# Optimization experiments

Hardware: AMD Instinct MI355X
Metric: run time of the kernel (lower is better)

The kernel has to match this reference:

```python
import jax, jax.numpy as jnp
import numpy as np

SH_C0 = 0.28209479177387814
EPS2D = 0.3      # gsplat low-pass filter added to 2D covariance diagonal
NEAR = 0.01
ALPHA_MIN = 1.0 / 255.0
ALPHA_MAX = 0.999


def setup_inputs() -> dict:
    key = jax.random.key(0)
    ks = jax.random.split(key, 5)
    N = 2048
    means = 0.1 * jax.random.normal(ks[0], (N, 3), jnp.float32)
    quats = jax.random.normal(ks[1], (N, 4), jnp.float32)
    scales = -2.3 + 0.3 * jax.random.normal(ks[2], (N, 3), jnp.float32)
    opacities = -1.0 + 0.5 * jax.random.normal(ks[3], (N,), jnp.float32)
    sh_coeffs = jax.random.normal(ks[4], (N, 1, 3), jnp.float32)
    viewmats = jnp.eye(4, dtype=jnp.float32).at[2, 3].set(2.0)[None]  # [1,4,4] world->cam
    Ks = jnp.array([[[150.0, 0.0, 64.0], [0.0, 150.0, 64.0], [0.0, 0.0, 1.0]]], jnp.float32)
    return dict(means=means, quats=quats, scales=scales, opacities=opacities,
                sh_coeffs=sh_coeffs, viewmats=viewmats, Ks=Ks, width=128, height=128)


def _splat_render(means, quats, scales, opacities, sh_coeffs, viewmats, Ks, width, height):
    # --- parameter activations (GaussianSplat.activated_parameters) ---
    quats = quats / jnp.linalg.norm(quats, axis=-1, keepdims=True)
    scales = jnp.minimum(jnp.exp(scales), 10.0)
    opac = jax.nn.sigmoid(opacities)                                  # [N]
    colors = jnp.maximum(sh_coeffs[:, 0, :] * SH_C0 + 0.5, 0.0)       # [N,3] sh_degree=0

    # --- 3D covariance from quaternion (w,x,y,z) and scale ---
    w, x, y, z = quats[:, 0], quats[:, 1], quats[:, 2], quats[:, 3]
    R = jnp.stack([
        1 - 2 * (y * y + z * z), 2 * (x * y - w * z), 2 * (x * z + w * y),
        2 * (x * y + w * z), 1 - 2 * (x * x + z * z), 2 * (y * z - w * x),
        2 * (x * z - w * y), 2 * (y * z + w * x), 1 - 2 * (x * x + y * y)],
        axis=-1).reshape(-1, 3, 3)                                    # [N,3,3]
    M = R * scales[:, None, :]                                        # R @ diag(s)
    cov3d = jnp.einsum('nij,nkj->nik', M, M)                          # [N,3,3]

    # --- project to camera frame ---
    Rcw = viewmats[:, :3, :3]                                         # [C,3,3]
    tcw = viewmats[:, :3, 3]                                          # [C,3]
    p_cam = jnp.einsum('cij,nj->cni', Rcw, means) + tcw[:, None, :]   # [C,N,3]
    Vc = jnp.einsum('cij,njk,clk->cnil', Rcw, cov3d, Rcw)             # [C,N,3,3]

    xc, yc, zc = p_cam[..., 0], p_cam[..., 1], p_cam[..., 2]
    valid = zc > NEAR
    zs = jnp.where(valid, zc, 1.0)
    rz = 1.0 / zs
    fx = Ks[:, 0, 0][:, None]; fy = Ks[:, 1, 1][:, None]
    cx = Ks[:, 0, 2][:, None]; cy = Ks[:, 1, 2][:, None]
    u = fx * xc * rz + cx                                             # [C,N]
    v = fy * yc * rz + cy

    # --- EWA 2D covariance: J Vc J^T + eps2d*I, J = d(proj)/d(p_cam) ---
    J00 = fx * rz; J02 = -fx * xc * rz * rz
    J11 = fy * rz; J12 = -fy * yc * rz * rz
    V00, V01, V02 = Vc[..., 0, 0], Vc[..., 0, 1], Vc[..., 0, 2]
    V11, V12, V22 = Vc[..., 1, 1], Vc[..., 1, 2], Vc[..., 2, 2]
    a = J00 * J00 * V00 + 2 * J00 * J02 * V02 + J02 * J02 * V22 + EPS2D
    b = J00 * (J11 * V01 + J12 * V02) + J02 * (J11 * V12 + J12 * V22)
    c = J11 * J11 * V11 + 2 * J11 * J12 * V12 + J12 * J12 * V22 + EPS2D
    det = a * c - b * b
    valid = valid & (det > 0)
    det_s = jnp.where(valid, det, 1.0)
    conA = c / det_s; conB = -b / det_s; conC = a / det_s             # conic (inverse cov)

    # --- per-pixel gaussian evaluation (pixel centers at +0.5) ---
    px = jnp.arange(width, dtype=jnp.float32) + 0.5                   # [W]
    py = jnp.arange(height, dtype=jnp.float32) + 0.5                  # [H]
    dx = px[None, None, :] - u[..., None]                             # [C,N,W]
    dy = py[None, None, :] - v[..., None]                             # [C,N,H]
    sigma = (0.5 * (conA[..., None, None] * (dx * dx)[:, :, None, :]
                    + conC[..., None, None] * (dy * dy)[..., None])
             + conB[..., None, None] * dy[..., None] * dx[:, :, None, :])  # [C,N,H,W]
    alpha = opac[None, :, None, None] * jnp.exp(-sigma)
    alpha = jnp.minimum(alpha, ALPHA_MAX)
    alpha = jnp.where(valid[..., None, None] & (alpha >= ALPHA_MIN), alpha, 0.0)

    # --- front-to-back alpha compositing in depth order ---
    order = jnp.argsort(jnp.where(valid, zc, jnp.inf), axis=1)        # [C,N]
    alpha_s = jnp.take_along_axis(alpha, order[:, :, None, None], axis=1)
    colors_s = jnp.take_along_axis(jnp.broadcast_to(colors[None], (alpha.shape[0],) + colors.shape),
                                   order[:, :, None], axis=1)         # [C,N,3]
    logT = jnp.cumsum(jnp.log1p(-alpha_s), axis=1)
    logT_excl = jnp.pad(logT, ((0, 0), (1, 0), (0, 0), (0, 0)))[:, :-1]
    weights = alpha_s * jnp.exp(logT_excl)                            # [C,N,H,W]
    img = jnp.einsum('cnhw,cnk->chwk', weights, colors_s)             # [C,H,W,3]
    return img


def reference(means, quats, scales, opacities, sh_coeffs, viewmats, Ks, width, height):
    return _splat_render(means, quats, scales, opacities, sh_coeffs, viewmats, Ks, width, height)
```

## Files before the change

kernel.cpp:

```cpp
#include <hip/hip_runtime.h>
#include <math.h>

#define SH_C0     0.28209479177387814f
#define EPS2D     0.3f
#define NEARZ     0.01f
#define ALPHA_MIN (1.0f/255.0f)
#define ALPHA_MAX 0.999f
#define LOG2E     1.4426950408889634f

#define LSEG    8
#define NLAYER  8
#define SEGS_R  (NLAYER * LSEG)
#define GSTRIDE 2052

__global__ __launch_bounds__(256) void prep_rank_kernel(
        const float* __restrict__ means,
        const float* __restrict__ quats,
        const float* __restrict__ scales,
        const float* __restrict__ opacities,
        const float* __restrict__ sh,
        const float* __restrict__ vm,
        const float* __restrict__ K,
        float* __restrict__ sorted,
        int N) {
    if (blockIdx.x == 0 && threadIdx.x < 12)
        sorted[12*(size_t)N + threadIdx.x] = 0.f;

    int wave = blockIdx.x * 4 + (threadIdx.x >> 6);
    int lane = threadIdx.x & 63;
    if (wave >= N) return;
    int i = wave;

    float r00=vm[0], r01=vm[1], r02=vm[2],  t0=vm[3];
    float r10=vm[4], r11=vm[5], r12=vm[6],  t1=vm[7];
    float r20=vm[8], r21=vm[9], r22=vm[10], t2=vm[11];

    float mx = means[3*i+0], my = means[3*i+1], mz = means[3*i+2];
    float zci = r20*mx + r21*my + r22*mz + t2;
    float keyi = (zci > NEARZ) ? zci : INFINITY;
    int cntk = 0;
    for (int j = lane; j < N; j += 64) {
        float ax = means[3*j+0], ay = means[3*j+1], az = means[3*j+2];
        float zcj = r20*ax + r21*ay + r22*az + t2;
        float keyj = (zcj > NEARZ) ? zcj : INFINITY;
        cntk += (keyj < keyi) || (keyj == keyi && j < i);
    }
    #pragma unroll
    for (int off = 32; off > 0; off >>= 1)
        cntk += __shfl_xor(cntk, off, 64);

    float qw = quats[4*i+0], qx = quats[4*i+1], qy = quats[4*i+2], qz = quats[4*i+3];
    float rqn = rsqrtf(qw*qw + qx*qx + qy*qy + qz*qz);
    qw *= rqn; qx *= rqn; qy *= rqn; qz *= rqn;

    float R00 = 1.f - 2.f*(qy*qy + qz*qz);
    float R01 = 2.f*(qx*qy - qw*qz);
    float R02 = 2.f*(qx*qz + qw*qy);
    float R10 = 2.f*(qx*qy + qw*qz);
    float R11 = 1.f - 2.f*(qx*qx + qz*qz);
    float R12 = 2.f*(qy*qz - qw*qx);
    float R20 = 2.f*(qx*qz - qw*qy);
    float R21 = 2.f*(qy*qz + qw*qx);
    float R22 = 1.f - 2.f*(qx*qx + qy*qy);

    float s0 = fminf(expf(scales[3*i+0]), 10.f);
    float s1 = fminf(expf(scales[3*i+1]), 10.f);
    float s2 = fminf(expf(scales[3*i+2]), 10.f);

    float M00=R00*s0, M01=R01*s1, M02=R02*s2;
    float M10=R10*s0, M11=R11*s1, M12=R12*s2;
    float M20=R20*s0, M21=R21*s1, M22=R22*s2;

    float c00 = M00*M00 + M01*M01 + M02*M02;
    float c01 = M00*M10 + M01*M11 + M02*M12;
    float c02 = M00*M20 + M01*M21 + M02*M22;
    float c11 = M10*M10 + M11*M11 + M12*M12;
    float c12 = M10*M20 + M11*M21 + M12*M22;
    float c22 = M20*M20 + M21*M21 + M22*M22;

    float xc = r00*mx + r01*my + r02*mz + t0;
    float yc = r10*mx + r11*my + r12*mz + t1;
    float zc = zci;

    float T00 = r00*c00 + r01*c01 + r02*c02;
    float T01 = r00*c01 + r01*c11 + r02*c12;
    float T02 = r00*c02 + r01*c12 + r02*c22;
    float T10 = r10*c00 + r11*c01 + r12*c02;
    float T11 = r10*c01 + r11*c11 + r12*c12;
    float T12 = r10*c02 + r11*c12 + r12*c22;
    float T20 = r20*c00 + r21*c01 + r22*c02;
    float T21 = r20*c01 + r21*c11 + r22*c12;
    float T22 = r20*c02 + r21*c12 + r22*c22;
    float V00 = T00*r00 + T01*r01 + T02*r02;
    float V01 = T00*r10 + T01*r11 + T02*r12;
    float V02 = T00*r20 + T01*r21 + T02*r22;
    float V11 = T10*r10 + T11*r11 + T12*r12;
    float V12 = T10*r20 + T11*r21 + T12*r22;
    float V22 = T20*r20 + T21*r21 + T22*r22;

    float fx = K[0], cx = K[2], fy = K[4], cy = K[5];

    bool valid = zc > NEARZ;
    float zs = valid ? zc : 1.0f;
    float rz = 1.0f / zs;
    float u = fx*xc*rz + cx;
    float v = fy*yc*rz + cy;
    float J00 = fx*rz;
    float J02 = -fx*xc*rz*rz;
    float J11 = fy*rz;
    float J12 = -fy*yc*rz*rz;

    float a = J00*J00*V00 + 2.f*J00*J02*V02 + J02*J02*V22 + EPS2D;
    float b = J00*(J11*V01 + J12*V02) + J02*(J11*V12 + J12*V22);
    float c = J11*J11*V11 + 2.f*J11*J12*V12 + J12*J12*V22 + EPS2D;
    float det = a*c - b*b;
    valid = valid && (det > 0.f);
    float det_s = valid ? det : 1.0f;
    float conA =  c / det_s;
    float conB = -b / det_s;
    float conC =  a / det_s;

    float op  = 1.0f / (1.0f + expf(-opacities[i]));
    float cr = fmaxf(sh[3*i+0]*SH_C0 + 0.5f, 0.f);
    float cg = fmaxf(sh[3*i+1]*SH_C0 + 0.5f, 0.f);
    float cb = fmaxf(sh[3*i+2]*SH_C0 + 0.5f, 0.f);

    float e0=0,e1=0,eA=0,eB=0,eC=0,eOp=0,eR=0,eG=0,eBc=0,rx=0,ry=0;
    if (valid) {
        float qmax = log2f(op * 255.f);
        if (qmax > 0.f) {
            float a2 = 0.5f*conA*LOG2E;
            float b2 = conB*LOG2E;
            float c2 = 0.5f*conC*LOG2E;
            float det2 = a2*c2 - 0.25f*b2*b2;
            float inv = qmax / det2;
            rx = sqrtf(c2 * inv) * 1.0001f + 0.01f;
            ry = sqrtf(a2 * inv) * 1.0001f + 0.01f;
            e0 = u; e1 = v; eA = a2; eB = b2; eC = c2; eOp = op;
            eR = cr; eG = cg; eBc = cb;
        }
    }

    if (lane < 12) {
        float val;
        switch (lane) {
            case 0:  val = e0;  break;
            case 1:  val = e1;  break;
            case 2:  val = rx;  break;
            case 3:  val = ry;  break;
            case 4:  val = eA;  break;
            case 5:  val = eB;  break;
            case 6:  val = eC;  break;
            case 7:  val = eOp; break;
            case 8:  val = eR;  break;
            case 9:  val = eG;  break;
            case 10: val = eBc; break;
            default: val = 0.f; break;
        }
        sorted[12*(size_t)cntk + lane] = val;
    }
}

__global__ __launch_bounds__(512) void cull_compact_kernel(
        const float* __restrict__ sorted,
        int* __restrict__ glist,
        int* __restrict__ lens,
        int N) {
    __shared__ int lbuf[8][256];
    __shared__ int lcnt[8];
    __shared__ int lbase[9];
    int tid  = threadIdx.x;
    int lane = tid & 63;
    int w    = tid >> 6;
    int t    = blockIdx.x;
    int tx = t & 15, ty = t >> 4;
    float x0 = (float)(tx * 8) + 0.5f, x1 = x0 + 7.f;
    float y0 = (float)(ty * 8) + 0.5f, y1 = y0 + 7.f;

    int chunkW = (N + 7) / 8;
    int gs = w * chunkW;
    int ge = min(gs + chunkW, N);

    int cnt = 0;
    for (int base = gs; base < ge; base += 64) {
        int gi = base + lane;
        int g  = min(gi, N - 1);
        const float4 h = *(const float4*)(sorted + 12*(size_t)g);
        bool hit = (gi < ge) &&
                   (h.y + h.w >= y0) && (h.y - h.w <= y1) &&
                   (h.x + h.z >= x0) && (h.x - h.z <= x1);
        unsigned long long m = __ballot(hit);
        int pos = cnt + __popcll(m & ((1ull << lane) - 1ull));
        if (hit) lbuf[w][pos] = gi;
        cnt += (int)__popcll(m);
    }
    if (lane == 0) lcnt[w] = cnt;
    __syncthreads();
    if (tid == 0) {
        int acc = 0;
        #pragma unroll
        for (int i = 0; i < 8; ++i) { lbase[i] = acc; acc += lcnt[i]; }
        lbase[8] = acc;
    }
    __syncthreads();
    int b = lbase[w];
    int* dst = glist + (size_t)t * GSTRIDE;
    for (int j = lane; j < cnt; j += 64) dst[b + j] = lbuf[w][j];
    int total = lbase[8];
    if (tid < 4)  dst[total + tid] = N;
    if (tid == 0) lens[t] = total;
}

__global__ __launch_bounds__(512, 4) void render_main_kernel(
        const float* __restrict__ sorted,
        const int* __restrict__ glist,
        const int* __restrict__ lens,
        float4* __restrict__ parts,
        int N, int P) {
    __shared__ float4 part[LSEG][64];
    int tid  = threadIdx.x;
    int lane = tid & 63;
    int w    = __builtin_amdgcn_readfirstlane(tid >> 6);
    int L    = blockIdx.x & (NLAYER - 1);
    int tile = blockIdx.x >> 3;
    int tx = tile & 15, ty = tile >> 4;
    float px = (float)(tx * 8 + (lane & 7)) + 0.5f;
    float py = (float)(ty * 8 + (lane >> 3)) + 0.5f;

    int len   = lens[tile];
    int chunk = (((len + SEGS_R - 1) / SEGS_R) + 3) & ~3;
    int s     = L * LSEG + w;
    int k0    = s * chunk;
    int lenp  = (len + 3) & ~3;
    int k1    = min(k0 + chunk, lenp);
    const int* lst = glist + (size_t)tile * GSTRIDE;

    float accr = 0.f, accg = 0.f, accb = 0.f, T = 1.f;
    for (int k = k0; k < k1; k += 4) {
        int4 gi = *(const int4*)(lst + k);
        int idx0 = gi.x, idx1 = gi.y, idx2 = gi.z, idx3 = gi.w;
        #pragma unroll
        for (int j = 0; j < 4; ++j) {
            int g = (j == 0) ? idx0 : (j == 1) ? idx1 : (j == 2) ? idx2 : idx3;
            const float4* rec = (const float4*)sorted + 3*(size_t)g;
            float4 r0 = rec[0];
            float4 r1 = rec[1];
            float4 r2 = rec[2];
            float dx = px - r0.x, dy = py - r0.y;
            float t2 = fmaf(r1.x, dx, r1.y * dy);
            float m  = dx * t2;
            float arg = fmaf(-r1.z, dy*dy, -m);
            float al = r1.w * __builtin_amdgcn_exp2f(arg);
            al = fminf(al, ALPHA_MAX);
            al = (al >= ALPHA_MIN) ? al : 0.f;
            float wgt = T * al;
            accr = fmaf(wgt, r2.x, accr);
            accg = fmaf(wgt, r2.y, accg);
            accb = fmaf(wgt, r2.z, accb);
            T = fmaf(-al, T, T);
        }
    }
    part[w][lane] = make_float4(accr, accg, accb, T);
    __syncthreads();

    if (tid < 64) {
        float R = 0.f, G = 0.f, Bc = 0.f, Tr = 1.f;
        #pragma unroll
        for (int ss = 0; ss < LSEG; ++ss) {
            float4 q = part[ss][tid];
            R  = fmaf(Tr, q.x, R);
            G  = fmaf(Tr, q.y, G);
            Bc = fmaf(Tr, q.z, Bc);
            Tr *= q.w;
        }
        int p = (ty * 8 + (tid >> 3)) * 128 + tx * 8 + (tid & 7);
        parts[(size_t)L * P + p] = make_float4(R, G, Bc, Tr);
    }
}

__global__ __launch_bounds__(256) void combine_kernel(
        const float4* __restrict__ parts,
        float* __restrict__ out, int P) {
    int p = blockIdx.x * 256 + threadIdx.x;
    if (p >= P) return;
    float R = 0.f, G = 0.f, B = 0.f, Tr = 1.f;
    #pragma unroll
    for (int l = 0; l < NLAYER; ++l) {
        float4 q = parts[(size_t)l * P + p];
        R  = fmaf(Tr, q.x, R);
        G  = fmaf(Tr, q.y, G);
        B  = fmaf(Tr, q.z, B);
        Tr *= q.w;
    }
    out[3*(size_t)p+0] = R;
    out[3*(size_t)p+1] = G;
    out[3*(size_t)p+2] = B;
}

extern "C" void kernel_launch(void* const* d_in, const int* in_sizes, int n_in,
                              void* d_out, int out_size, void* d_ws, size_t ws_size,
                              hipStream_t stream) {
    const float* means     = (const float*)d_in[0];
    const float* quats     = (const float*)d_in[1];
    const float* scales    = (const float*)d_in[2];
    const float* opacities = (const float*)d_in[3];
    const float* sh        = (const float*)d_in[4];
    const float* vm        = (const float*)d_in[5];
    const float* K         = (const float*)d_in[6];

    int N = in_sizes[0] / 3;
    int P = out_size / 3;
    int tiles = P / 64;

    float*  sorted = (float*)d_ws;
    int*    glist  = (int*)(sorted + (size_t)(N + 1) * 12);
    int*    lens   = glist + (size_t)tiles * GSTRIDE;
    float4* parts  = (float4*)(lens + tiles);

    prep_rank_kernel<<<(N + 3) / 4, 256, 0, stream>>>(
        means, quats, scales, opacities, sh, vm, K, sorted, N);
    cull_compact_kernel<<<tiles, 512, 0, stream>>>(
        sorted, glist, lens, N);
    render_main_kernel<<<tiles * NLAYER, 512, 0, stream>>>(
        sorted, glist, lens, parts, N, P);
    combine_kernel<<<(P + 255) / 256, 256, 0, stream>>>(
        parts, (float*)d_out, P);
}
```

Baseline: 92.06 us.

## Fuse per-tile culling into render kernel and cache depth keys in LDS

The separate cull/compact kernel is removed. Each render wave now culls its own contiguous slice of depth-sorted Gaussians against the tile bounds, using a compact float4 header array written by the prep kernel, and builds its hit list in shared memory. The prep kernel computes all depth keys once into shared memory instead of every wave recomputing them from global means, and it uses 512-thread blocks. Layers per tile drop from 8 to 4. This saves a kernel launch and the global list round trip, but it hardcodes N ≤ 2048 and bounds each wave's list at 72 entries.

```diff
diff --git a/kernel.cpp b/kernel.cpp
--- a/kernel.cpp
+++ b/kernel.cpp
@@ -8,12 +8,12 @@
 #define ALPHA_MAX 0.999f
 #define LOG2E     1.4426950408889634f
 
+#define NLAYER  4
 #define LSEG    8
-#define NLAYER  8
-#define SEGS_R  (NLAYER * LSEG)
-#define GSTRIDE 2052
-
-__global__ __launch_bounds__(256) void prep_rank_kernel(
+#define WSTRIDE 72
+#define MAXN    2048
+
+__global__ __launch_bounds__(512) void prep_rank_kernel(
         const float* __restrict__ means,
         const float* __restrict__ quats,
         const float* __restrict__ scales,
@@ -22,33 +22,40 @@
         const float* __restrict__ vm,
         const float* __restrict__ K,
         float* __restrict__ sorted,
+        float4* __restrict__ hdr,
         int N) {
-    if (blockIdx.x == 0 && threadIdx.x < 12)
-        sorted[12*(size_t)N + threadIdx.x] = 0.f;
-
-    int wave = blockIdx.x * 4 + (threadIdx.x >> 6);
-    int lane = threadIdx.x & 63;
-    if (wave >= N) return;
-    int i = wave;
+    __shared__ float kbuf[MAXN];
+    int tid = threadIdx.x;
 
     float r00=vm[0], r01=vm[1], r02=vm[2],  t0=vm[3];
     float r10=vm[4], r11=vm[5], r12=vm[6],  t1=vm[7];
     float r20=vm[8], r21=vm[9], r22=vm[10], t2=vm[11];
 
-    float mx = means[3*i+0], my = means[3*i+1], mz = means[3*i+2];
-    float zci = r20*mx + r21*my + r22*mz + t2;
-    float keyi = (zci > NEARZ) ? zci : INFINITY;
+    for (int j = tid; j < N; j += 512) {
+        float zc = r20*means[3*j+0] + r21*means[3*j+1] + r22*means[3*j+2] + t2;
+        kbuf[j] = (zc > NEARZ) ? zc : INFINITY;
+    }
+    __syncthreads();
+
+    if (blockIdx.x == 0 && tid < 12)
+        sorted[12*(size_t)N + tid] = 0.f;
+
+    int lane = tid & 63;
+    int w    = tid >> 6;
+    int i    = blockIdx.x * 8 + w;
+    if (i >= N) return;
+
+    float keyi = kbuf[i];
     int cntk = 0;
     for (int j = lane; j < N; j += 64) {
-        float ax = means[3*j+0], ay = means[3*j+1], az = means[3*j+2];
-        float zcj = r20*ax + r21*ay + r22*az + t2;
-        float keyj = (zcj > NEARZ) ? zcj : INFINITY;
-        cntk += (keyj < keyi) || (keyj == keyi && j < i);
+        float kj = kbuf[j];
+        cntk += (kj < keyi) || (kj == keyi && j < i);
     }
     #pragma unroll
     for (int off = 32; off > 0; off >>= 1)
         cntk += __shfl_xor(cntk, off, 64);
 
+    float mx = means[3*i+0], my = means[3*i+1], mz = means[3*i+2];
     float qw = quats[4*i+0], qx = quats[4*i+1], qy = quats[4*i+2], qz = quats[4*i+3];
     float rqn = rsqrtf(qw*qw + qx*qx + qy*qy + qz*qz);
     qw *= rqn; qx *= rqn; qy *= rqn; qz *= rqn;
@@ -80,7 +87,6 @@
 
     float xc = r00*mx + r01*my + r02*mz + t0;
     float yc = r10*mx + r11*my + r12*mz + t1;
-    float zc = zci;
 
     float T00 = r00*c00 + r01*c01 + r02*c02;
     float T01 = r00*c01 + r01*c11 + r02*c12;
@@ -100,9 +106,9 @@
 
     float fx = K[0], cx = K[2], fy = K[4], cy = K[5];
 
-    bool valid = zc > NEARZ;
-    float zs = valid ? zc : 1.0f;
-    float rz = 1.0f / zs;
+    bool valid = keyi < INFINITY;
+    float zc = valid ? keyi : 1.0f;
+    float rz = 1.0f / zc;
     float u = fx*xc*rz + cx;
     float v = fy*yc*rz + cy;
     float J00 = fx*rz;
@@ -159,89 +165,56 @@
         }
         sorted[12*(size_t)cntk + lane] = val;
     }
-}
-
-__global__ __launch_bounds__(512) void cull_compact_kernel(
+    if (lane == 0)
+        hdr[cntk] = make_float4(e0, e1, rx, ry);
+}
+
+__global__ __launch_bounds__(512, 8) void render_kernel(
         const float* __restrict__ sorted,
-        int* __restrict__ glist,
-        int* __restrict__ lens,
-        int N) {
-    __shared__ int lbuf[8][256];
-    __shared__ int lcnt[8];
-    __shared__ int lbase[9];
-    int tid  = threadIdx.x;
-    int lane = tid & 63;
-    int w    = tid >> 6;
-    int t    = blockIdx.x;
-    int tx = t & 15, ty = t >> 4;
-    float x0 = (float)(tx * 8) + 0.5f, x1 = x0 + 7.f;
-    float y0 = (float)(ty * 8) + 0.5f, y1 = y0 + 7.f;
-
-    int chunkW = (N + 7) / 8;
-    int gs = w * chunkW;
-    int ge = min(gs + chunkW, N);
-
-    int cnt = 0;
-    for (int base = gs; base < ge; base += 64) {
-        int gi = base + lane;
-        int g  = min(gi, N - 1);
-        const float4 h = *(const float4*)(sorted + 12*(size_t)g);
-        bool hit = (gi < ge) &&
-                   (h.y + h.w >= y0) && (h.y - h.w <= y1) &&
-                   (h.x + h.z >= x0) && (h.x - h.z <= x1);
-        unsigned long long m = __ballot(hit);
-        int pos = cnt + __popcll(m & ((1ull << lane) - 1ull));
-        if (hit) lbuf[w][pos] = gi;
-        cnt += (int)__popcll(m);
-    }
-    if (lane == 0) lcnt[w] = cnt;
-    __syncthreads();
-    if (tid == 0) {
-        int acc = 0;
-        #pragma unroll
-        for (int i = 0; i < 8; ++i) { lbase[i] = acc; acc += lcnt[i]; }
-        lbase[8] = acc;
-    }
-    __syncthreads();
-    int b = lbase[w];
-    int* dst = glist + (size_t)t * GSTRIDE;
-    for (int j = lane; j < cnt; j += 64) dst[b + j] = lbuf[w][j];
-    int total = lbase[8];
-    if (tid < 4)  dst[total + tid] = N;
-    if (tid == 0) lens[t] = total;
-}
-
-__global__ __launch_bounds__(512, 4) void render_main_kernel(
-        const float* __restrict__ sorted,
-        const int* __restrict__ glist,
-        const int* __restrict__ lens,
+        const float4* __restrict__ hdr,
         float4* __restrict__ parts,
         int N, int P) {
+    __shared__ __align__(16) int lbuf[LSEG * WSTRIDE];
     __shared__ float4 part[LSEG][64];
     int tid  = threadIdx.x;
     int lane = tid & 63;
     int w    = __builtin_amdgcn_readfirstlane(tid >> 6);
     int L    = blockIdx.x & (NLAYER - 1);
-    int tile = blockIdx.x >> 3;
+    int tile = blockIdx.x >> 2;
     int tx = tile & 15, ty = tile >> 4;
-    float px = (float)(tx * 8 + (lane & 7)) + 0.5f;
-    float py = (float)(ty * 8 + (lane >> 3)) + 0.5f;
-
-    int len   = lens[tile];
-    int chunk = (((len + SEGS_R - 1) / SEGS_R) + 3) & ~3;
-    int s     = L * LSEG + w;
-    int k0    = s * chunk;
-    int lenp  = (len + 3) & ~3;
-    int k1    = min(k0 + chunk, lenp);
-    const int* lst = glist + (size_t)tile * GSTRIDE;
+    float x0 = (float)(tx * 8) + 0.5f, x1 = x0 + 7.f;
+    float y0 = (float)(ty * 8) + 0.5f, y1 = y0 + 7.f;
+    float px = x0 + (float)(lane & 7);
+    float py = y0 + (float)(lane >> 3);
+
+    int chunkB = (N + NLAYER - 1) / NLAYER;
+    int cw     = (chunkB + LSEG - 1) / LSEG;
+    int lend   = min((L + 1) * chunkB, N);
+    int gs     = L * chunkB + w * cw;
+    int ge     = min(gs + cw, lend);
+    int* lw    = lbuf + w * WSTRIDE;
+
+    int cnt = 0;
+    for (int base = gs; base < ge; base += 64) {
+        int gi = base + lane;
+        float4 h = hdr[min(gi, N - 1)];
+        bool hit = (gi < ge) &&
+                   (h.y + h.w >= y0) && (h.y - h.w <= y1) &&
+                   (h.x + h.z >= x0) && (h.x - h.z <= x1);
+        unsigned long long m = __ballot(hit);
+        int pos = cnt + (int)__popcll(m & ((1ull << lane) - 1ull));
+        if (hit) lw[pos] = gi;
+        cnt += (int)__popcll(m);
+    }
+    int cpad = (cnt + 3) & ~3;
+    if (lane < cpad - cnt) lw[cnt + lane] = N;
 
     float accr = 0.f, accg = 0.f, accb = 0.f, T = 1.f;
-    for (int k = k0; k < k1; k += 4) {
-        int4 gi = *(const int4*)(lst + k);
-        int idx0 = gi.x, idx1 = gi.y, idx2 = gi.z, idx3 = gi.w;
+    for (int k = 0; k < cpad; k += 4) {
+        int4 gi4 = *(const int4*)(lw + k);
         #pragma unroll
         for (int j = 0; j < 4; ++j) {
-            int g = (j == 0) ? idx0 : (j == 1) ? idx1 : (j == 2) ? idx2 : idx3;
+            int g = (j == 0) ? gi4.x : (j == 1) ? gi4.y : (j == 2) ? gi4.z : gi4.w;
             const float4* rec = (const float4*)sorted + 3*(size_t)g;
             float4 r0 = rec[0];
             float4 r1 = rec[1];
@@ -313,16 +286,13 @@
     int tiles = P / 64;
 
     float*  sorted = (float*)d_ws;
-    int*    glist  = (int*)(sorted + (size_t)(N + 1) * 12);
-    int*    lens   = glist + (size_t)tiles * GSTRIDE;
-    float4* parts  = (float4*)(lens + tiles);
-
-    prep_rank_kernel<<<(N + 3) / 4, 256, 0, stream>>>(
-        means, quats, scales, opacities, sh, vm, K, sorted, N);
-    cull_compact_kernel<<<tiles, 512, 0, stream>>>(
-        sorted, glist, lens, N);
-    render_main_kernel<<<tiles * NLAYER, 512, 0, stream>>>(
-        sorted, glist, lens, parts, N, P);
+    float4* hdr    = (float4*)(sorted + (size_t)(N + 1) * 12);
+    float4* parts  = hdr + N;
+
+    prep_rank_kernel<<<(N + 7) / 8, 512, 0, stream>>>(
+        means, quats, scales, opacities, sh, vm, K, sorted, hdr, N);
+    render_kernel<<<tiles * NLAYER, 512, 0, stream>>>(
+        sorted, hdr, parts, N, P);
     combine_kernel<<<(P + 255) / 256, 256, 0, stream>>>(
         parts, (float*)d_out, P);
 }
```

Result: faster. 87.69 us (-4.7%).
